# Optimization experiments

Measured on AMD Instinct MI355X. Metric: run time of the kernel, lower is better.

## Reference

```python
import jax, jax.numpy as jnp
import numpy as np

HEADS = 16
NUM_MEM_KV = 16
SPARSE_TOPK = 8


def setup_inputs() -> dict:
    key = jax.random.key(0)
    ks = jax.random.split(key, 10)
    b, n, dim = 2, 2048, 1024
    h, dh = HEADS, 64
    inner = h * dh
    s = 0.02
    return {
        "x": jax.random.normal(ks[0], (b, n, dim), jnp.float32),
        "Wq": jax.random.normal(ks[1], (dim, inner), jnp.float32) * s,
        "Wk": jax.random.normal(ks[2], (dim, inner), jnp.float32) * s,
        "Wv": jax.random.normal(ks[3], (dim, inner), jnp.float32) * s,
        "pre_proj": jax.random.normal(ks[4], (h, h), jnp.float32),
        "post_proj": jax.random.normal(ks[5], (h, h), jnp.float32),
        "mem_k": jax.random.normal(ks[6], (h, NUM_MEM_KV, dh), jnp.float32),
        "mem_v": jax.random.normal(ks[7], (h, NUM_MEM_KV, dh), jnp.float32),
        "Wo": jax.random.normal(ks[8], (inner, dim), jnp.float32) * s,
        "bo": jnp.zeros((dim,), jnp.float32),
    }


def reference(x, Wq, Wk, Wv, pre_proj, post_proj, mem_k, mem_v, Wo, bo):
    b, n, dim = x.shape
    h = HEADS
    dh = Wq.shape[1] // h
    nm = mem_k.shape[1]
    scale = dh ** -0.5

    def split_heads(t):  # [b, n, h*dh] -> [b, h, n, dh]
        return t.reshape(b, -1, h, dh).transpose(0, 2, 1, 3)

    q = split_heads(x @ Wq)
    k = split_heads(x @ Wk)
    v = split_heads(x @ Wv)

    # prepend learned memory key/values: j = nm + n
    k = jnp.concatenate([jnp.broadcast_to(mem_k[None], (b, h, nm, dh)), k], axis=2)
    v = jnp.concatenate([jnp.broadcast_to(mem_v[None], (b, h, nm, dh)), v], axis=2)

    dots = jnp.einsum("bhid,bhjd->bhij", q, k) * scale  # [b, h, n, nm+n]
    mask_value = -jnp.finfo(dots.dtype).max

    # talking heads (pre-softmax): mix across the head dimension
    dots = jnp.einsum("bhij,hk->bkij", dots, pre_proj)

    # causal mask, shifted by nm mem slots (mem positions always visible)
    j = nm + n
    causal = jnp.arange(n)[:, None] < (jnp.arange(j)[None, :] - nm)  # True = masked
    dots = jnp.where(causal[None, None], mask_value, dots)

    # sparse top-k pruning along the key axis
    top = jax.lax.top_k(dots, SPARSE_TOPK)[0]
    thresh = top[..., -1:]
    dots = jnp.where(dots < thresh, mask_value, dots)

    attn = jax.nn.softmax(dots, axis=-1)

    # talking heads (post-softmax)
    attn = jnp.einsum("bhij,hk->bkij", attn, post_proj)

    out = jnp.einsum("bhij,bhjd->bhid", attn, v)
    out = out.transpose(0, 2, 1, 3).reshape(b, n, h * dh)
    return out @ Wo + bo
```

## Files before the change

kernel.cpp:

```cpp
#include <hip/hip_runtime.h>
#include <hip/hip_bf16.h>

typedef unsigned short u16;
typedef unsigned int   u32;

#define BB   2
#define NN   2048
#define HS   16
#define DH   64
#define NM   16
#define JT   2064
#define DIM  1024
#define CT   26
#define JC   5

#define SPLITSZ ((size_t)BB * HS * JT * DH)

__device__ __forceinline__ float bfval(u16 u) { return __uint_as_float(((u32)u) << 16); }
__device__ __forceinline__ float lo16(u32 u)  { return __uint_as_float(u << 16); }
__device__ __forceinline__ float hi16(u32 u)  { return __uint_as_float(u & 0xffff0000u); }
__device__ __forceinline__ u16 f2bf(float f)
{
    __hip_bfloat16 h = __float2bfloat16(f);
    return *(u16*)&h;
}

typedef __bf16 bf16x8 __attribute__((ext_vector_type(8)));
typedef float  f32x4  __attribute__((ext_vector_type(4)));

__global__ void prep_mem_kernel(const float* __restrict__ mem_k, u16* __restrict__ k_sp)
{
    int t = blockIdx.x * 256 + threadIdx.x;
    int d = t & 63, j = (t >> 6) & 15, h = (t >> 10) & 15, b = (t >> 14) & 1;
    float x = mem_k[(h * NM + j) * DH + d];
    size_t di = ((size_t)(b * HS + h) * JT + j) * DH + d;
    u16 sh = f2bf(x);
    float d1 = x - bfval(sh);
    u16 sm = f2bf(d1);
    u16 sl = f2bf(d1 - bfval(sm));
    k_sp[di] = sh; k_sp[di + SPLITSZ] = sm; k_sp[di + 2 * SPLITSZ] = sl;
}

__global__ void prep_wot_kernel(const float* __restrict__ Wo, u16* __restrict__ wot)
{
    int t = blockIdx.x * 256 + threadIdx.x;
    int k = t & 1023, n = t >> 10;
    wot[(size_t)n * 1024 + k] = f2bf(Wo[(size_t)k * 1024 + n]);
}

__global__ __launch_bounds__(256) void gemm_kernel(
    const float* __restrict__ A, const float* __restrict__ Bw,
    u16* __restrict__ dst16, float* __restrict__ dstf, int mode)
{
    __shared__ __align__(16) u16 a_h[128][32];
    __shared__ __align__(16) u16 a_m[128][32];
    __shared__ __align__(16) u16 a_l[128][32];
    __shared__ __align__(16) u16 b_hT[64][32];
    __shared__ __align__(16) u16 b_mT[64][32];
    __shared__ __align__(16) u16 b_lT[64][32];

    const int tid  = threadIdx.x;
    const int m0   = blockIdx.x * 128;
    const int n0   = blockIdx.y * 64;
    const int wave = tid >> 6, lane = tid & 63;
    const int ln16 = lane & 15, quad = lane >> 4;

    const int arow = tid >> 1;
    const int ac   = (tid & 1) * 16;
    const int brow = tid >> 3;
    const int bc   = (tid & 7) * 8;

    f32x4 acc[8] = {};

    for (int k0 = 0; k0 < 1024; k0 += 32) {
        float av[16];
        {
            const float4* ap = (const float4*)&A[(size_t)(m0 + arow) * 1024 + k0 + ac];
            *(float4*)&av[0]  = ap[0]; *(float4*)&av[4]  = ap[1];
            *(float4*)&av[8]  = ap[2]; *(float4*)&av[12] = ap[3];
        }
        float bv[8];
        {
            const float4* bp = (const float4*)&Bw[(size_t)(k0 + brow) * 1024 + n0 + bc];
            *(float4*)&bv[0] = bp[0]; *(float4*)&bv[4] = bp[1];
        }
        u16 ah[16], am[16], al[16], bh[8], bm[8], bl[8];
        #pragma unroll
        for (int e = 0; e < 16; ++e) {
            ah[e] = f2bf(av[e]);
            float d1 = av[e] - bfval(ah[e]);
            am[e] = f2bf(d1);
            al[e] = f2bf(d1 - bfval(am[e]));
        }
        #pragma unroll
        for (int e = 0; e < 8; ++e) {
            bh[e] = f2bf(bv[e]);
            float d1 = bv[e] - bfval(bh[e]);
            bm[e] = f2bf(d1);
            bl[e] = f2bf(d1 - bfval(bm[e]));
        }
        __syncthreads();
        *(uint4*)&a_h[arow][ac]     = ((uint4*)ah)[0];
        *(uint4*)&a_h[arow][ac + 8] = ((uint4*)ah)[1];
        *(uint4*)&a_m[arow][ac]     = ((uint4*)am)[0];
        *(uint4*)&a_m[arow][ac + 8] = ((uint4*)am)[1];
        *(uint4*)&a_l[arow][ac]     = ((uint4*)al)[0];
        *(uint4*)&a_l[arow][ac + 8] = ((uint4*)al)[1];
        #pragma unroll
        for (int e = 0; e < 8; ++e) {
            b_hT[bc + e][brow] = bh[e];
            b_mT[bc + e][brow] = bm[e];
            b_lT[bc + e][brow] = bl[e];
        }
        __syncthreads();

        bf16x8 a0h = *(const bf16x8*)&a_h[wave * 32 + ln16][quad * 8];
        bf16x8 a0m = *(const bf16x8*)&a_m[wave * 32 + ln16][quad * 8];
        bf16x8 a0l = *(const bf16x8*)&a_l[wave * 32 + ln16][quad * 8];
        bf16x8 a1h = *(const bf16x8*)&a_h[wave * 32 + 16 + ln16][quad * 8];
        bf16x8 a1m = *(const bf16x8*)&a_m[wave * 32 + 16 + ln16][quad * 8];
        bf16x8 a1l = *(const bf16x8*)&a_l[wave * 32 + 16 + ln16][quad * 8];
        #pragma unroll
        for (int c = 0; c < 4; ++c) {
            bf16x8 bh_ = *(const bf16x8*)&b_hT[c * 16 + ln16][quad * 8];
            bf16x8 bm_ = *(const bf16x8*)&b_mT[c * 16 + ln16][quad * 8];
            bf16x8 bl_ = *(const bf16x8*)&b_lT[c * 16 + ln16][quad * 8];
            acc[c]     = __builtin_amdgcn_mfma_f32_16x16x32_bf16(a0m, bm_, acc[c],     0, 0, 0);
            acc[c]     = __builtin_amdgcn_mfma_f32_16x16x32_bf16(a0h, bl_, acc[c],     0, 0, 0);
            acc[c]     = __builtin_amdgcn_mfma_f32_16x16x32_bf16(a0l, bh_, acc[c],     0, 0, 0);
            acc[c]     = __builtin_amdgcn_mfma_f32_16x16x32_bf16(a0h, bm_, acc[c],     0, 0, 0);
            acc[c]     = __builtin_amdgcn_mfma_f32_16x16x32_bf16(a0m, bh_, acc[c],     0, 0, 0);
            acc[c]     = __builtin_amdgcn_mfma_f32_16x16x32_bf16(a0h, bh_, acc[c],     0, 0, 0);
            acc[4 + c] = __builtin_amdgcn_mfma_f32_16x16x32_bf16(a1m, bm_, acc[4 + c], 0, 0, 0);
            acc[4 + c] = __builtin_amdgcn_mfma_f32_16x16x32_bf16(a1h, bl_, acc[4 + c], 0, 0, 0);
            acc[4 + c] = __builtin_amdgcn_mfma_f32_16x16x32_bf16(a1l, bh_, acc[4 + c], 0, 0, 0);
            acc[4 + c] = __builtin_amdgcn_mfma_f32_16x16x32_bf16(a1h, bm_, acc[4 + c], 0, 0, 0);
            acc[4 + c] = __builtin_amdgcn_mfma_f32_16x16x32_bf16(a1m, bh_, acc[4 + c], 0, 0, 0);
            acc[4 + c] = __builtin_amdgcn_mfma_f32_16x16x32_bf16(a1h, bh_, acc[4 + c], 0, 0, 0);
        }
    }

    #pragma unroll
    for (int hf = 0; hf < 2; ++hf) {
        #pragma unroll
        for (int c = 0; c < 4; ++c) {
            #pragma unroll
            for (int r = 0; r < 4; ++r) {
                int row = m0 + wave * 32 + hf * 16 + quad * 4 + r;
                int col = n0 + c * 16 + ln16;
                float v = acc[hf * 4 + c][r];
                if (mode == 1) {
                    dstf[(size_t)row * 1024 + col] = v;
                } else {
                    int b = row >> 11, i = row & 2047;
                    int hd = col >> 6, d = col & 63;
                    if (mode == 0) {
                        dst16[(((size_t)(b * HS + hd)) * NN + i) * DH + d] = f2bf(v);
                    } else {
                        size_t di = (((size_t)(b * HS + hd)) * JT + NM + i) * DH + d;
                        u16 sh = f2bf(v);
                        float d1 = v - bfval(sh);
                        u16 sm = f2bf(d1);
                        u16 sl = f2bf(d1 - bfval(sm));
                        dst16[di] = sh;
                        dst16[di + SPLITSZ] = sm;
                        dst16[di + 2 * SPLITSZ] = sl;
                    }
                }
            }
        }
    }
}

__global__ __launch_bounds__(512) void score_topk_kernel(
    const u16* __restrict__ k_hi, const u16* __restrict__ k_mi,
    const u16* __restrict__ k_lo,
    const float* __restrict__ q_all, const float* __restrict__ pre,
    float* __restrict__ ws_val, u16* __restrict__ ws_idx)
{
    const int jc = blockIdx.x;
    const int iy = 127 - blockIdx.y;
    const int b  = blockIdx.z;
    const int ntiles = iy + 2;
    const int jt_lo = jc * CT;
    if (jt_lo >= ntiles) return;
    const int jt_hi = min(jt_lo + CT, ntiles);

    __shared__ __align__(16) float fsm[8448];
    float* S  = fsm;
    float* pp = fsm + 8192;

    const int tid  = threadIdx.x;
    const int i0   = iy * 16;
    const int wave = tid >> 6, lane = tid & 63;
    const int ln16 = lane & 15, quad = lane >> 4;

    if (tid < 256) pp[tid] = pre[tid] * 0.125f;

    bf16x8 qh[2][2], qm[2][2], ql[2][2];
    {
        const float* qrow = q_all + (size_t)(b * NN + i0 + ln16) * DIM;
        #pragma unroll
        for (int h2 = 0; h2 < 2; ++h2) {
            const int h = wave * 2 + h2;
            #pragma unroll
            for (int half = 0; half < 2; ++half) {
                const float* src = qrow + h * 64 + half * 32 + quad * 8;
                float4 u0 = *(const float4*)src;
                float4 u1 = *(const float4*)(src + 4);
                float xv[8] = {u0.x, u0.y, u0.z, u0.w, u1.x, u1.y, u1.z, u1.w};
                u16 eh[8], em[8], el[8];
                #pragma unroll
                for (int e = 0; e < 8; ++e) {
                    eh[e] = f2bf(xv[e]);
                    float d1 = xv[e] - bfval(eh[e]);
                    em[e] = f2bf(d1);
                    el[e] = f2bf(d1 - bfval(em[e]));
                }
                qh[h2][half] = *(bf16x8*)eh;
                qm[h2][half] = *(bf16x8*)em;
                ql[h2][half] = *(bf16x8*)el;
            }
        }
    }
    __syncthreads();

    const int kk_r = (wave & 3) * 4 + (lane & 3);
    const int ti_r = lane >> 2;
    const int tjh  = wave >> 2;

    float pw[16];
    #pragma unroll
    for (int h = 0; h < 16; ++h) pw[h] = pp[h * 16 + kk_r];

    float tv[8];
    int   tx[8];
    #pragma unroll
    for (int t = 0; t < 8; ++t) { tv[t] = -1e30f; tx[t] = 0; }
    const int jlim = NM + i0 + ti_r;

    const u32 kbase0 = ((u32)(b * HS) * JT + (u32)ln16) * DH + (u32)(quad * 8);

    for (int jt = jt_lo; jt < jt_hi; ++jt) {
        float* Sb = S + ((jt - jt_lo) & 1) * 4096;

        #pragma unroll
        for (int h2 = 0; h2 < 2; ++h2) {
            const int h = wave * 2 + h2;
            const u32 koff = kbase0 + (u32)h * (JT * DH) + (u32)(jt * 16) * DH;
            f32x4 acc = {};
            #pragma unroll
            for (int half = 0; half < 2; ++half) {
                const u32 ko = koff + (u32)(half * 32);
                bf16x8 kh_ = *(const bf16x8*)(k_hi + ko);
                bf16x8 km_ = *(const bf16x8*)(k_mi + ko);
                bf16x8 kl_ = *(const bf16x8*)(k_lo + ko);
                acc = __builtin_amdgcn_mfma_f32_16x16x32_bf16(qm[h2][half], km_, acc, 0, 0, 0);
                acc = __builtin_amdgcn_mfma_f32_16x16x32_bf16(qh[h2][half], kl_, acc, 0, 0, 0);
                acc = __builtin_amdgcn_mfma_f32_16x16x32_bf16(ql[h2][half], kh_, acc, 0, 0, 0);
                acc = __builtin_amdgcn_mfma_f32_16x16x32_bf16(qh[h2][half], km_, acc, 0, 0, 0);
                acc = __builtin_amdgcn_mfma_f32_16x16x32_bf16(qm[h2][half], kh_, acc, 0, 0, 0);
                acc = __builtin_amdgcn_mfma_f32_16x16x32_bf16(qh[h2][half], kh_, acc, 0, 0, 0);
            }
            #pragma unroll
            for (int r = 0; r < 4; ++r) {
                int i   = quad * 4 + r;
                int rot = ((ln16 >> 2) + i + (i >> 2)) & 3;
                Sb[h * 256 + i * 16 + rot * 4 + (ln16 & 3)] = acc[r];
            }
        }
        __syncthreads();

        const int jb = jt * 16;
        #pragma unroll
        for (int tc = 0; tc < 2; ++tc) {
            const int tjc = tjh * 2 + tc;
            const int rot = (tjc + ti_r + (ti_r >> 2)) & 3;
            const float* sp = Sb + ti_r * 16 + rot * 4;
            float m0 = 0.f, m1 = 0.f, m2 = 0.f, m3 = 0.f;
            #pragma unroll
            for (int h = 0; h < 16; ++h) {
                float4 s = *(const float4*)(sp + h * 256);
                m0 += pw[h] * s.x; m1 += pw[h] * s.y;
                m2 += pw[h] * s.z; m3 += pw[h] * s.w;
            }
            const int jb2 = jb + tjc * 4;
            #pragma unroll
            for (int e = 0; e < 4; ++e) {
                float c = (e == 0) ? m0 : (e == 1) ? m1 : (e == 2) ? m2 : m3;
                int j = jb2 + e;
                if (j <= jlim && c > tv[7]) {
                    #pragma unroll
                    for (int t = 7; t >= 1; --t) {
                        if (c > tv[t - 1])      { tv[t] = tv[t - 1]; tx[t] = tx[t - 1]; }
                        else if (c > tv[t])     { tv[t] = c;         tx[t] = j; }
                    }
                    if (c > tv[0]) { tv[0] = c; tx[0] = j; }
                }
            }
        }
    }

    __syncthreads();
    const int row = kk_r * 16 + ti_r;
    if (tjh == 1) {
        #pragma unroll
        for (int t = 0; t < 8; ++t) {
            fsm[row * 8 + t]        = tv[t];
            fsm[4096 + row * 8 + t] = __int_as_float(tx[t]);
        }
    }
    __syncthreads();
    if (tjh == 0) {
        #pragma unroll
        for (int t2 = 0; t2 < 8; ++t2) {
            float c = fsm[row * 8 + t2];
            int   j = __float_as_int(fsm[4096 + row * 8 + t2]);
            if (c > tv[7]) {
                #pragma unroll
                for (int t = 7; t >= 1; --t) {
                    if (c > tv[t - 1])      { tv[t] = tv[t - 1]; tx[t] = tx[t - 1]; }
                    else if (c > tv[t])     { tv[t] = c;         tx[t] = j; }
                }
                if (c > tv[0]) { tv[0] = c; tx[0] = j; }
            }
        }
        size_t base = ((((size_t)b * HS + kk_r) * NN + i0 + ti_r) * JC + jc) * 8;
        #pragma unroll
        for (int t = 0; t < 8; ++t) {
            ws_val[base + t] = tv[t];
            ws_idx[base + t] = (u16)tx[t];
        }
    }
}

__global__ __launch_bounds__(256) void merge_pv_kernel(
    const u16* __restrict__ v_bf, const float* __restrict__ mem_v,
    const float* __restrict__ ws_val, const u16* __restrict__ ws_idx,
    const float* __restrict__ post, const u16* __restrict__ wot,
    const float* __restrict__ bo, float* __restrict__ out)
{
    __shared__ __align__(16) float fsm[13312];
    float* dotsm = fsm + 8704;
    float* pp2   = fsm + 13056;
    u16*   arows = (u16*)fsm;

    const int tid = threadIdx.x;
    const int b   = blockIdx.y;
    const int i0  = blockIdx.x * 16;
    const int ntiles = blockIdx.x + 2;
    const int jc_cnt = (ntiles + CT - 1) / CT;

    pp2[tid] = post[tid];

    const int kk_r = tid & 15, ti_r = tid >> 4;

    float tv[8];
    int   tx[8];
    #pragma unroll
    for (int t = 0; t < 8; ++t) { tv[t] = -1e30f; tx[t] = 0; }

    size_t rbase = (((size_t)b * HS + kk_r) * NN + i0 + ti_r) * JC;
    for (int jc = 0; jc < jc_cnt; ++jc) {
        #pragma unroll
        for (int t2 = 0; t2 < 8; ++t2) {
            float c = ws_val[(rbase + jc) * 8 + t2];
            int   j = ws_idx[(rbase + jc) * 8 + t2];
            if (c > tv[7]) {
                #pragma unroll
                for (int t = 7; t >= 1; --t) {
                    if (c > tv[t - 1])      { tv[t] = tv[t - 1]; tx[t] = tx[t - 1]; }
                    else if (c > tv[t])     { tv[t] = c;         tx[t] = j; }
                }
                if (c > tv[0]) { tv[0] = c; tx[0] = j; }
            }
        }
    }

    float m = tv[0];
    float wv[8], wsum = 0.f;
    #pragma unroll
    for (int t = 0; t < 8; ++t) { wv[t] = __expf(tv[t] - m); wsum += wv[t]; }
    float inv = 1.f / wsum;

    #pragma unroll
    for (int t = 0; t < 8; ++t) {
        dotsm[(kk_r * 16 + ti_r) * 8 + t]        = wv[t] * inv;
        dotsm[2048 + (kk_r * 16 + ti_r) * 8 + t] = __int_as_float(tx[t]);
    }
    __syncthreads();

    const int ti_o = tid >> 4, k2 = tid & 15;
    {
        float acc[64];
        #pragma unroll
        for (int d = 0; d < 64; ++d) acc[d] = 0.f;
        const u16*   vws_base  = v_bf  + (size_t)(b * HS + k2) * NN * DH;
        const float* vmem_base = mem_v + (size_t)k2 * NM * DH;

        for (int kk = 0; kk < 16; ++kk) {
            float p2 = pp2[kk * 16 + k2];
            for (int t = 0; t < 8; ++t) {
                float w = dotsm[(kk * 16 + ti_o) * 8 + t] * p2;
                int j = __float_as_int(dotsm[2048 + (kk * 16 + ti_o) * 8 + t]);
                if (j < NM) {
                    const float* vr = vmem_base + (size_t)j * DH;
                    #pragma unroll
                    for (int r = 0; r < 16; ++r) {
                        float4 u = *(const float4*)&vr[r * 4];
                        acc[r * 4 + 0] += w * u.x; acc[r * 4 + 1] += w * u.y;
                        acc[r * 4 + 2] += w * u.z; acc[r * 4 + 3] += w * u.w;
                    }
                } else {
                    const uint4* vr = (const uint4*)(vws_base + (size_t)(j - NM) * DH);
                    #pragma unroll
                    for (int r = 0; r < 8; ++r) {
                        uint4 u = vr[r];
                        acc[r * 8 + 0] += w * lo16(u.x); acc[r * 8 + 1] += w * hi16(u.x);
                        acc[r * 8 + 2] += w * lo16(u.y); acc[r * 8 + 3] += w * hi16(u.y);
                        acc[r * 8 + 4] += w * lo16(u.z); acc[r * 8 + 5] += w * hi16(u.z);
                        acc[r * 8 + 6] += w * lo16(u.w); acc[r * 8 + 7] += w * hi16(u.w);
                    }
                }
            }
        }
        #pragma unroll
        for (int d = 0; d < 64; ++d) {
            float o = acc[d];
            o = (o == o) ? o : 1e4f;
            arows[ti_o * 1032 + k2 * 64 + d] = f2bf(o);
        }
    }
    __syncthreads();

    const int wave = tid >> 6, lane = tid & 63;
    const int ln16 = lane & 15, quad = lane >> 4;

    f32x4 oacc[16];
    #pragma unroll
    for (int t = 0; t < 16; ++t) {
        float bv = bo[(t * 4 + wave) * 16 + ln16];
        oacc[t][0] = bv; oacc[t][1] = bv; oacc[t][2] = bv; oacc[t][3] = bv;
    }

    for (int k0 = 0; k0 < 1024; k0 += 32) {
        bf16x8 af = *(const bf16x8*)&arows[ln16 * 1032 + k0 + quad * 8];
        #pragma unroll
        for (int t = 0; t < 16; ++t) {
            const int n = (t * 4 + wave) * 16 + ln16;
            bf16x8 bf_ = *(const bf16x8*)&wot[(size_t)n * 1024 + k0 + quad * 8];
            oacc[t] = __builtin_amdgcn_mfma_f32_16x16x32_bf16(af, bf_, oacc[t], 0, 0, 0);
        }
    }

    #pragma unroll
    for (int t = 0; t < 16; ++t) {
        const int n = (t * 4 + wave) * 16 + ln16;
        #pragma unroll
        for (int r = 0; r < 4; ++r) {
            int row = quad * 4 + r;
            out[(size_t)(b * NN + i0 + row) * DIM + n] = oacc[t][r];
        }
    }
}

extern "C" void kernel_launch(void* const* d_in, const int* in_sizes, int n_in,
                              void* d_out, int out_size, void* d_ws, size_t ws_size,
                              hipStream_t stream)
{
    (void)in_sizes; (void)n_in; (void)out_size; (void)ws_size;
    const float* x     = (const float*)d_in[0];
    const float* Wq    = (const float*)d_in[1];
    const float* Wk    = (const float*)d_in[2];
    const float* Wv    = (const float*)d_in[3];
    const float* pre   = (const float*)d_in[4];
    const float* post  = (const float*)d_in[5];
    const float* mem_k = (const float*)d_in[6];
    const float* mem_v = (const float*)d_in[7];
    const float* Wo    = (const float*)d_in[8];
    const float* bo    = (const float*)d_in[9];

    u16*   k_sp   = (u16*)d_ws;
    u16*   v_bf   = k_sp + 3 * SPLITSZ;
    float* ws_val = (float*)(v_bf + (size_t)BB * HS * NN * DH);
    u16*   ws_idx = (u16*)(ws_val + (size_t)BB * HS * NN * JC * 8);
    u16*   wot    = ws_idx + (size_t)BB * HS * NN * JC * 8;
    float* q_tmp  = (float*)d_out;

    prep_mem_kernel<<<128, 256, 0, stream>>>(mem_k, k_sp);
    prep_wot_kernel<<<4096, 256, 0, stream>>>(Wo, wot);

    dim3 gg(32, 16);
    gemm_kernel<<<gg, 256, 0, stream>>>(x, Wq, nullptr, q_tmp, 1);
    gemm_kernel<<<gg, 256, 0, stream>>>(x, Wk, k_sp, nullptr, 2);
    gemm_kernel<<<gg, 256, 0, stream>>>(x, Wv, v_bf, nullptr, 0);

    dim3 gs(JC, 128, 2);
    score_topk_kernel<<<gs, 512, 0, stream>>>(k_sp, k_sp + SPLITSZ,
                                              k_sp + 2 * SPLITSZ,
                                              (const float*)d_out,
                                              pre, ws_val, ws_idx);

    dim3 ga(128, 2);
    merge_pv_kernel<<<ga, 256, 0, stream>>>(v_bf, mem_v, ws_val, ws_idx,
                                            post, wot, bo, (float*)d_out);
}
```

Before: 1.153 ms.

## Balance causal score/top-k work with equal-size linear tile ranges per block

Replaces the 3D grid of fixed 26-tile chunks per query row, which leaves many idle or partly filled blocks under the causal triangle, with 512 persistent blocks. Each block takes an equal contiguous range of the flattened triangular tile sequence and may span several query rows, writing partial top-k results into per-row slots. The merge kernel recomputes how many slots each row has from the same partition. This evens out per-block load, at the cost of reloading and splitting Q at each row boundary and extra index arithmetic.

```diff
diff --git a/kernel.cpp b/kernel.cpp
--- a/kernel.cpp
+++ b/kernel.cpp
@@ -11,8 +11,9 @@
 #define NM   16
 #define JT   2064
 #define DIM  1024
-#define CT   26
 #define JC   5
+#define NBB  256
+#define TOTT 8384
 
 #define SPLITSZ ((size_t)BB * HS * JT * DH)
 
@@ -24,6 +25,16 @@
     __hip_bfloat16 h = __float2bfloat16(f);
     return *(u16*)&h;
 }
+
+__device__ __forceinline__ int blk_start(int k) { return (131 * k) >> 2; }
+__device__ __forceinline__ int blk_of(int g)
+{
+    int k = (4 * g) / 131;
+    while (blk_start(k + 1) <= g) ++k;
+    while (blk_start(k) > g) --k;
+    return k;
+}
+__device__ __forceinline__ int row_start(int iy) { return (iy * (iy + 3)) >> 1; }
 
 typedef __bf16 bf16x8 __attribute__((ext_vector_type(8)));
 typedef float  f32x4  __attribute__((ext_vector_type(4)));
@@ -178,118 +189,158 @@
     const float* __restrict__ q_all, const float* __restrict__ pre,
     float* __restrict__ ws_val, u16* __restrict__ ws_idx)
 {
-    const int jc = blockIdx.x;
-    const int iy = 127 - blockIdx.y;
-    const int b  = blockIdx.z;
-    const int ntiles = iy + 2;
-    const int jt_lo = jc * CT;
-    if (jt_lo >= ntiles) return;
-    const int jt_hi = min(jt_lo + CT, ntiles);
-
-    __shared__ __align__(16) float fsm[8448];
-    float* S  = fsm;
-    float* pp = fsm + 8192;
+    const int bid = blockIdx.x;
+    const int b   = bid >> 8;
+    const int kb  = (bid & 7) * 32 + ((bid & 255) >> 3);
+
+    int g = blk_start(kb);
+    const int gend = blk_start(kb + 1);
+
+    __shared__ __align__(16) float fsm[12544];
+    float* S   = fsm;
+    float* pp  = fsm + 8192;
+    float* scr = fsm + 8448;
 
     const int tid  = threadIdx.x;
-    const int i0   = iy * 16;
     const int wave = tid >> 6, lane = tid & 63;
     const int ln16 = lane & 15, quad = lane >> 4;
 
     if (tid < 256) pp[tid] = pre[tid] * 0.125f;
-
-    bf16x8 qh[2][2], qm[2][2], ql[2][2];
-    {
-        const float* qrow = q_all + (size_t)(b * NN + i0 + ln16) * DIM;
-        #pragma unroll
-        for (int h2 = 0; h2 < 2; ++h2) {
-            const int h = wave * 2 + h2;
-            #pragma unroll
-            for (int half = 0; half < 2; ++half) {
-                const float* src = qrow + h * 64 + half * 32 + quad * 8;
-                float4 u0 = *(const float4*)src;
-                float4 u1 = *(const float4*)(src + 4);
-                float xv[8] = {u0.x, u0.y, u0.z, u0.w, u1.x, u1.y, u1.z, u1.w};
-                u16 eh[8], em[8], el[8];
-                #pragma unroll
-                for (int e = 0; e < 8; ++e) {
-                    eh[e] = f2bf(xv[e]);
-                    float d1 = xv[e] - bfval(eh[e]);
-                    em[e] = f2bf(d1);
-                    el[e] = f2bf(d1 - bfval(em[e]));
-                }
-                qh[h2][half] = *(bf16x8*)eh;
-                qm[h2][half] = *(bf16x8*)em;
-                ql[h2][half] = *(bf16x8*)el;
-            }
-        }
-    }
     __syncthreads();
 
     const int kk_r = (wave & 3) * 4 + (lane & 3);
     const int ti_r = lane >> 2;
     const int tjh  = wave >> 2;
+    const int srow = kk_r * 16 + ti_r;
 
     float pw[16];
     #pragma unroll
     for (int h = 0; h < 16; ++h) pw[h] = pp[h * 16 + kk_r];
 
-    float tv[8];
-    int   tx[8];
-    #pragma unroll
-    for (int t = 0; t < 8; ++t) { tv[t] = -1e30f; tx[t] = 0; }
-    const int jlim = NM + i0 + ti_r;
-
     const u32 kbase0 = ((u32)(b * HS) * JT + (u32)ln16) * DH + (u32)(quad * 8);
 
-    for (int jt = jt_lo; jt < jt_hi; ++jt) {
-        float* Sb = S + ((jt - jt_lo) & 1) * 4096;
-
-        #pragma unroll
-        for (int h2 = 0; h2 < 2; ++h2) {
-            const int h = wave * 2 + h2;
-            const u32 koff = kbase0 + (u32)h * (JT * DH) + (u32)(jt * 16) * DH;
-            f32x4 acc = {};
-            #pragma unroll
-            for (int half = 0; half < 2; ++half) {
-                const u32 ko = koff + (u32)(half * 32);
-                bf16x8 kh_ = *(const bf16x8*)(k_hi + ko);
-                bf16x8 km_ = *(const bf16x8*)(k_mi + ko);
-                bf16x8 kl_ = *(const bf16x8*)(k_lo + ko);
-                acc = __builtin_amdgcn_mfma_f32_16x16x32_bf16(qm[h2][half], km_, acc, 0, 0, 0);
-                acc = __builtin_amdgcn_mfma_f32_16x16x32_bf16(qh[h2][half], kl_, acc, 0, 0, 0);
-                acc = __builtin_amdgcn_mfma_f32_16x16x32_bf16(ql[h2][half], kh_, acc, 0, 0, 0);
-                acc = __builtin_amdgcn_mfma_f32_16x16x32_bf16(qh[h2][half], km_, acc, 0, 0, 0);
-                acc = __builtin_amdgcn_mfma_f32_16x16x32_bf16(qm[h2][half], kh_, acc, 0, 0, 0);
-                acc = __builtin_amdgcn_mfma_f32_16x16x32_bf16(qh[h2][half], kh_, acc, 0, 0, 0);
-            }
-            #pragma unroll
-            for (int r = 0; r < 4; ++r) {
-                int i   = quad * 4 + r;
-                int rot = ((ln16 >> 2) + i + (i >> 2)) & 3;
-                Sb[h * 256 + i * 16 + rot * 4 + (ln16 & 3)] = acc[r];
-            }
-        }
+    int iy = (int)((sqrtf((float)(8 * g + 9)) - 3.0f) * 0.5f);
+    while (row_start(iy + 1) <= g) ++iy;
+    while (row_start(iy) > g) --iy;
+
+    while (g < gend) {
+        const int ntiles = iy + 2;
+        const int Srow0  = row_start(iy);
+        int jt = g - Srow0;
+        const int nrow   = min(ntiles - jt, gend - g);
+        const int jt_hi  = jt + nrow;
+        const int i0     = iy * 16;
+        const int slot   = kb - blk_of(Srow0);
+
+        bf16x8 qh[2][2], qm[2][2], ql[2][2];
+        {
+            const float* qrow = q_all + (size_t)(b * NN + i0 + ln16) * DIM;
+            #pragma unroll
+            for (int h2 = 0; h2 < 2; ++h2) {
+                const int h = wave * 2 + h2;
+                #pragma unroll
+                for (int half = 0; half < 2; ++half) {
+                    const float* src = qrow + h * 64 + half * 32 + quad * 8;
+                    float4 u0 = *(const float4*)src;
+                    float4 u1 = *(const float4*)(src + 4);
+                    float xv[8] = {u0.x, u0.y, u0.z, u0.w, u1.x, u1.y, u1.z, u1.w};
+                    u16 eh[8], em[8], el[8];
+                    #pragma unroll
+                    for (int e = 0; e < 8; ++e) {
+                        eh[e] = f2bf(xv[e]);
+                        float d1 = xv[e] - bfval(eh[e]);
+                        em[e] = f2bf(d1);
+                        el[e] = f2bf(d1 - bfval(em[e]));
+                    }
+                    qh[h2][half] = *(bf16x8*)eh;
+                    qm[h2][half] = *(bf16x8*)em;
+                    ql[h2][half] = *(bf16x8*)el;
+                }
+            }
+        }
+
+        float tv[8];
+        int   tx[8];
+        #pragma unroll
+        for (int t = 0; t < 8; ++t) { tv[t] = -1e30f; tx[t] = 0; }
+        const int jlim = NM + i0 + ti_r;
+
+        int par = 0;
+        for (; jt < jt_hi; ++jt, par ^= 1) {
+            float* Sb = S + par * 4096;
+
+            #pragma unroll
+            for (int h2 = 0; h2 < 2; ++h2) {
+                const int h = wave * 2 + h2;
+                const u32 koff = kbase0 + (u32)h * (JT * DH) + (u32)(jt * 16) * DH;
+                f32x4 acc = {};
+                #pragma unroll
+                for (int half = 0; half < 2; ++half) {
+                    const u32 ko = koff + (u32)(half * 32);
+                    bf16x8 kh_ = *(const bf16x8*)(k_hi + ko);
+                    bf16x8 km_ = *(const bf16x8*)(k_mi + ko);
+                    bf16x8 kl_ = *(const bf16x8*)(k_lo + ko);
+                    acc = __builtin_amdgcn_mfma_f32_16x16x32_bf16(qm[h2][half], km_, acc, 0, 0, 0);
+                    acc = __builtin_amdgcn_mfma_f32_16x16x32_bf16(qh[h2][half], kl_, acc, 0, 0, 0);
+                    acc = __builtin_amdgcn_mfma_f32_16x16x32_bf16(ql[h2][half], kh_, acc, 0, 0, 0);
+                    acc = __builtin_amdgcn_mfma_f32_16x16x32_bf16(qh[h2][half], km_, acc, 0, 0, 0);
+                    acc = __builtin_amdgcn_mfma_f32_16x16x32_bf16(qm[h2][half], kh_, acc, 0, 0, 0);
+                    acc = __builtin_amdgcn_mfma_f32_16x16x32_bf16(qh[h2][half], kh_, acc, 0, 0, 0);
+                }
+                #pragma unroll
+                for (int r = 0; r < 4; ++r) {
+                    int i   = quad * 4 + r;
+                    int rot = ((ln16 >> 2) + i + (i >> 2)) & 3;
+                    Sb[h * 256 + i * 16 + rot * 4 + (ln16 & 3)] = acc[r];
+                }
+            }
+            __syncthreads();
+
+            const int jb = jt * 16;
+            #pragma unroll
+            for (int tc = 0; tc < 2; ++tc) {
+                const int tjc = tjh * 2 + tc;
+                const int rot = (tjc + ti_r + (ti_r >> 2)) & 3;
+                const float* sp = Sb + ti_r * 16 + rot * 4;
+                float m0 = 0.f, m1 = 0.f, m2 = 0.f, m3 = 0.f;
+                #pragma unroll
+                for (int h = 0; h < 16; ++h) {
+                    float4 s4 = *(const float4*)(sp + h * 256);
+                    m0 += pw[h] * s4.x; m1 += pw[h] * s4.y;
+                    m2 += pw[h] * s4.z; m3 += pw[h] * s4.w;
+                }
+                const int jb2 = jb + tjc * 4;
+                #pragma unroll
+                for (int e = 0; e < 4; ++e) {
+                    float c = (e == 0) ? m0 : (e == 1) ? m1 : (e == 2) ? m2 : m3;
+                    int j = jb2 + e;
+                    if (j <= jlim && c > tv[7]) {
+                        #pragma unroll
+                        for (int t = 7; t >= 1; --t) {
+                            if (c > tv[t - 1])      { tv[t] = tv[t - 1]; tx[t] = tx[t - 1]; }
+                            else if (c > tv[t])     { tv[t] = c;         tx[t] = j; }
+                        }
+                        if (c > tv[0]) { tv[0] = c; tx[0] = j; }
+                    }
+                }
+            }
+        }
+
         __syncthreads();
-
-        const int jb = jt * 16;
-        #pragma unroll
-        for (int tc = 0; tc < 2; ++tc) {
-            const int tjc = tjh * 2 + tc;
-            const int rot = (tjc + ti_r + (ti_r >> 2)) & 3;
-            const float* sp = Sb + ti_r * 16 + rot * 4;
-            float m0 = 0.f, m1 = 0.f, m2 = 0.f, m3 = 0.f;
-            #pragma unroll
-            for (int h = 0; h < 16; ++h) {
-                float4 s = *(const float4*)(sp + h * 256);
-                m0 += pw[h] * s.x; m1 += pw[h] * s.y;
-                m2 += pw[h] * s.z; m3 += pw[h] * s.w;
-            }
-            const int jb2 = jb + tjc * 4;
-            #pragma unroll
-            for (int e = 0; e < 4; ++e) {
-                float c = (e == 0) ? m0 : (e == 1) ? m1 : (e == 2) ? m2 : m3;
-                int j = jb2 + e;
-                if (j <= jlim && c > tv[7]) {
+        if (tjh == 1) {
+            #pragma unroll
+            for (int t = 0; t < 8; ++t) {
+                scr[srow * 8 + t]        = tv[t];
+                scr[2048 + srow * 8 + t] = __int_as_float(tx[t]);
+            }
+        }
+        __syncthreads();
+        if (tjh == 0) {
+            #pragma unroll
+            for (int t2 = 0; t2 < 8; ++t2) {
+                float c = scr[srow * 8 + t2];
+                int   j = __float_as_int(scr[2048 + srow * 8 + t2]);
+                if (c > tv[7]) {
                     #pragma unroll
                     for (int t = 7; t >= 1; --t) {
                         if (c > tv[t - 1])      { tv[t] = tv[t - 1]; tx[t] = tx[t - 1]; }
@@ -298,39 +349,16 @@
                     if (c > tv[0]) { tv[0] = c; tx[0] = j; }
                 }
             }
-        }
-    }
-
-    __syncthreads();
-    const int row = kk_r * 16 + ti_r;
-    if (tjh == 1) {
-        #pragma unroll
-        for (int t = 0; t < 8; ++t) {
-            fsm[row * 8 + t]        = tv[t];
-            fsm[4096 + row * 8 + t] = __int_as_float(tx[t]);
-        }
-    }
-    __syncthreads();
-    if (tjh == 0) {
-        #pragma unroll
-        for (int t2 = 0; t2 < 8; ++t2) {
-            float c = fsm[row * 8 + t2];
-            int   j = __float_as_int(fsm[4096 + row * 8 + t2]);
-            if (c > tv[7]) {
-                #pragma unroll
-                for (int t = 7; t >= 1; --t) {
-                    if (c > tv[t - 1])      { tv[t] = tv[t - 1]; tx[t] = tx[t - 1]; }
-                    else if (c > tv[t])     { tv[t] = c;         tx[t] = j; }
-                }
-                if (c > tv[0]) { tv[0] = c; tx[0] = j; }
-            }
-        }
-        size_t base = ((((size_t)b * HS + kk_r) * NN + i0 + ti_r) * JC + jc) * 8;
-        #pragma unroll
-        for (int t = 0; t < 8; ++t) {
-            ws_val[base + t] = tv[t];
-            ws_idx[base + t] = (u16)tx[t];
-        }
+            size_t base = ((((size_t)b * HS + kk_r) * NN + i0 + ti_r) * JC + slot) * 8;
+            #pragma unroll
+            for (int t = 0; t < 8; ++t) {
+                ws_val[base + t] = tv[t];
+                ws_idx[base + t] = (u16)tx[t];
+            }
+        }
+
+        g += nrow;
+        ++iy;
     }
 }
 
@@ -349,7 +377,8 @@
     const int b   = blockIdx.y;
     const int i0  = blockIdx.x * 16;
     const int ntiles = blockIdx.x + 2;
-    const int jc_cnt = (ntiles + CT - 1) / CT;
+    const int Srow0  = row_start(blockIdx.x);
+    const int jc_cnt = blk_of(Srow0 + ntiles - 1) - blk_of(Srow0) + 1;
 
     pp2[tid] = post[tid];
 
@@ -495,11 +524,10 @@
     gemm_kernel<<<gg, 256, 0, stream>>>(x, Wk, k_sp, nullptr, 2);
     gemm_kernel<<<gg, 256, 0, stream>>>(x, Wv, v_bf, nullptr, 0);
 
-    dim3 gs(JC, 128, 2);
-    score_topk_kernel<<<gs, 512, 0, stream>>>(k_sp, k_sp + SPLITSZ,
-                                              k_sp + 2 * SPLITSZ,
-                                              (const float*)d_out,
-                                              pre, ws_val, ws_idx);
+    score_topk_kernel<<<512, 512, 0, stream>>>(k_sp, k_sp + SPLITSZ,
+                                               k_sp + 2 * SPLITSZ,
+                                               (const float*)d_out,
+                                               pre, ws_val, ws_idx);
 
     dim3 ga(128, 2);
     merge_pv_kernel<<<ga, 256, 0, stream>>>(v_bf, mem_v, ws_val, ws_idx,
```

Measured after the change: 1.057 ms. 1.09x faster.
